# Kernel optimization log

Hardware: AMD Instinct MI355X
Metric: run time of the kernel (lower is better)

Reference implementation:

```python
import jax, jax.numpy as jnp
import numpy as np

D_MODEL = 512
NUM_HEADS = 8
D_K = D_MODEL // NUM_HEADS
SCALE = D_K ** (-0.5)
B, L = 2, 256


def _tropical_linear(x, W, b):
    # max-plus linear: y[..., o] = max_i (x[..., i] + W[o, i]) + b[o]
    # x: (B, L, Din), W: (Dout, Din)
    return jnp.max(x[:, :, None, :] + W[None, None, :, :], axis=-1) + b


def _split_heads(t):
    Bn, Ln, Dn = t.shape
    return t.reshape(Bn, Ln, NUM_HEADS, D_K).transpose(0, 2, 1, 3)  # (B,H,L,dk)


def setup_inputs() -> dict:
    key = jax.random.key(0)
    ks = jax.random.split(key, 8)
    s = 1.0 / np.sqrt(D_MODEL)
    return {
        "x": jax.random.normal(ks[0], (B, L, D_MODEL), jnp.float32),
        "qW": jax.random.normal(ks[1], (D_MODEL, D_MODEL), jnp.float32) * s,
        "qb": jnp.zeros((D_MODEL,), jnp.float32),
        "kW": jax.random.normal(ks[2], (D_MODEL, D_MODEL), jnp.float32) * s,
        "kb": jnp.zeros((D_MODEL,), jnp.float32),
        "vW": jax.random.normal(ks[3], (D_MODEL, D_MODEL), jnp.float32) * s,
        "vb": jnp.zeros((D_MODEL,), jnp.float32),
        "oW": jax.random.normal(ks[4], (D_MODEL, D_MODEL), jnp.float32) * s,
        "ob": jnp.zeros((D_MODEL,), jnp.float32),
        "gW": jnp.zeros((NUM_HEADS, D_MODEL), jnp.float32),  # torch init: zeros
        "gb": jnp.full((NUM_HEADS,), 2.0, jnp.float32),      # torch init: +2.0
        "temp": jnp.ones((NUM_HEADS,), jnp.float32),
    }


def reference(x, qW, qb, kW, kb, vW, vb, oW, ob, gW, gb, temp):
    Bn, Ln, Dn = x.shape
    Q = _split_heads(_tropical_linear(x, qW, qb))  # (B,H,L,dk)
    K = _split_heads(_tropical_linear(x, kW, kb))
    V = _split_heads(x @ vW.T + vb)

    class_scores = jnp.einsum('bhqd,bhkd->bhqk', Q, K) * SCALE
    # tropical max-plus scores: max_d (Q[q,d] + K[k,d])
    trop_scores = jnp.max(Q[:, :, :, None, :] + K[:, :, None, :, :], axis=-1) * SCALE

    g = jax.nn.sigmoid(x @ gW.T + gb)            # (B,L,H)
    g = g.transpose(0, 2, 1)[..., None]          # (B,H,L,1)
    scores = g * trop_scores + (1.0 - g) * class_scores

    # Maslov temperature softmax: per-head learnable temperature
    attn = jax.nn.softmax(scores / temp[None, :, None, None], axis=-1)

    out = jnp.einsum('bhqk,bhkd->bhqd', attn, V)
    out = out.transpose(0, 2, 1, 3).reshape(Bn, Ln, Dn)
    return out @ oW.T + ob, attn
```

## Files before the change

### kernel.cpp

```cpp
#include <hip/hip_runtime.h>
#include <math.h>

#define DM    512
#define LSEQ  256
#define NB    2
#define NH    8
#define DK    64
#define SCALEF 0.125f
#define KC    64

__global__ __launch_bounds__(256) void qkvg_kernel(
    const float* __restrict__ x,
    const float* __restrict__ qW, const float* __restrict__ qb,
    const float* __restrict__ kW, const float* __restrict__ kb,
    const float* __restrict__ vW, const float* __restrict__ vb,
    const float* __restrict__ gW, const float* __restrict__ gb,
    float* __restrict__ Qo, float* __restrict__ Ko,
    float* __restrict__ Vo, float* __restrict__ go)
{
    const int tid = threadIdx.x;
    const int bx  = blockIdx.x;

    if (bx >= 192) {
        const int gx  = bx - 192;
        const int row = gx * 32 + (tid >> 3);
        const int h   = tid & 7;
        const float4* xr = (const float4*)(x  + row * DM);
        const float4* wr = (const float4*)(gW + h  * DM);
        float acc = 0.f;
        #pragma unroll 8
        for (int i = 0; i < DM / 4; ++i) {
            float4 a = xr[i], w = wr[i];
            acc = fmaf(a.x, w.x, acc);
            acc = fmaf(a.y, w.y, acc);
            acc = fmaf(a.z, w.z, acc);
            acc = fmaf(a.w, w.w, acc);
        }
        acc += gb[h];
        go[row * NH + h] = 1.f / (1.f + __expf(-acc));
        return;
    }

    const int rt = bx / 24;
    const int ct = bx % 24;
    const int op = ct >> 3;
    const int row0  = rt * 64;
    const int col0m = (ct & 7) * 64;

    const float* __restrict__ W;
    const float* __restrict__ bias;
    float* __restrict__ out;
    bool trop;
    if      (op == 0) { W = qW; bias = qb; out = Qo; trop = true;  }
    else if (op == 1) { W = kW; bias = kb; out = Ko; trop = true;  }
    else              { W = vW; bias = vb; out = Vo; trop = false; }

    __shared__ float Xs[KC][68];
    __shared__ float Ws[KC][68];

    const int ty = tid >> 4, tx = tid & 15;
    const int sr = tid & 63;
    const int sq = tid >> 6;

    const float* xp = x + (row0  + sr) * DM + sq * 16;
    const float* wp = W + (col0m + sr) * DM + sq * 16;

    float4 xg[4], wg[4];
    #pragma unroll
    for (int i = 0; i < 4; ++i) {
        xg[i] = *(const float4*)(xp + i * 4);
        wg[i] = *(const float4*)(wp + i * 4);
    }

    const float init = trop ? -INFINITY : 0.f;
    float acc[4][4];
    #pragma unroll
    for (int i = 0; i < 4; ++i)
        #pragma unroll
        for (int j = 0; j < 4; ++j) acc[i][j] = init;

    for (int k0 = 0; k0 < DM; k0 += KC) {
        __syncthreads();
        #pragma unroll
        for (int i = 0; i < 4; ++i) {
            const int kk = sq * 16 + i * 4;
            Xs[kk + 0][sr] = xg[i].x;  Xs[kk + 1][sr] = xg[i].y;
            Xs[kk + 2][sr] = xg[i].z;  Xs[kk + 3][sr] = xg[i].w;
            Ws[kk + 0][sr] = wg[i].x;  Ws[kk + 1][sr] = wg[i].y;
            Ws[kk + 2][sr] = wg[i].z;  Ws[kk + 3][sr] = wg[i].w;
        }
        __syncthreads();
        if (k0 + KC < DM) {
            #pragma unroll
            for (int i = 0; i < 4; ++i) {
                xg[i] = *(const float4*)(xp + k0 + KC + i * 4);
                wg[i] = *(const float4*)(wp + k0 + KC + i * 4);
            }
        }
        if (trop) {
            #pragma unroll 4
            for (int kp = 0; kp < KC / 2; ++kp) {
                const int kk = kp * 2;
                float4 x0 = *(const float4*)&Xs[kk    ][ty * 4];
                float4 x1 = *(const float4*)&Xs[kk + 1][ty * 4];
                float4 w0 = *(const float4*)&Ws[kk    ][tx * 4];
                float4 w1 = *(const float4*)&Ws[kk + 1][tx * 4];
                const float xa0[4] = {x0.x, x0.y, x0.z, x0.w};
                const float xa1[4] = {x1.x, x1.y, x1.z, x1.w};
                const float wa0[4] = {w0.x, w0.y, w0.z, w0.w};
                const float wa1[4] = {w1.x, w1.y, w1.z, w1.w};
                #pragma unroll
                for (int i = 0; i < 4; ++i)
                    #pragma unroll
                    for (int j = 0; j < 4; ++j)
                        acc[i][j] = fmaxf(fmaxf(acc[i][j], xa0[i] + wa0[j]),
                                          xa1[i] + wa1[j]);
            }
        } else {
            #pragma unroll 4
            for (int kp = 0; kp < KC / 2; ++kp) {
                const int kk = kp * 2;
                float4 x0 = *(const float4*)&Xs[kk    ][ty * 4];
                float4 x1 = *(const float4*)&Xs[kk + 1][ty * 4];
                float4 w0 = *(const float4*)&Ws[kk    ][tx * 4];
                float4 w1 = *(const float4*)&Ws[kk + 1][tx * 4];
                const float xa0[4] = {x0.x, x0.y, x0.z, x0.w};
                const float xa1[4] = {x1.x, x1.y, x1.z, x1.w};
                const float wa0[4] = {w0.x, w0.y, w0.z, w0.w};
                const float wa1[4] = {w1.x, w1.y, w1.z, w1.w};
                #pragma unroll
                for (int i = 0; i < 4; ++i)
                    #pragma unroll
                    for (int j = 0; j < 4; ++j) {
                        acc[i][j] = fmaf(xa0[i], wa0[j], acc[i][j]);
                        acc[i][j] = fmaf(xa1[i], wa1[j], acc[i][j]);
                    }
            }
        }
    }

    const float4 bv = *(const float4*)&bias[col0m + tx * 4];
    #pragma unroll
    for (int i = 0; i < 4; ++i) {
        const int r = row0 + ty * 4 + i;
        float4 o = make_float4(acc[i][0] + bv.x, acc[i][1] + bv.y,
                               acc[i][2] + bv.z, acc[i][3] + bv.w);
        *(float4*)&out[(size_t)r * DM + col0m + tx * 4] = o;
    }
}

__global__ __launch_bounds__(256) void attn_kernel(
    const float* __restrict__ Q, const float* __restrict__ K,
    const float* __restrict__ V, const float* __restrict__ g,
    const float* __restrict__ temp,
    float* __restrict__ attn_out, float* __restrict__ hout)
{
    const int tid = threadIdx.x;
    const int bh  = blockIdx.y;
    const int b   = bh >> 3, h = bh & 7;
    const int q0  = blockIdx.x * 16;
    const int ty  = tid >> 4, tx = tid & 15;

    __shared__ float Kd[64][68];
    __shared__ float Vs[64][68];
    __shared__ float Ss[16][260];

    const float* qrow = Q + (size_t)(b * LSEQ + q0 + ty) * DM + h * DK;
    float4 qreg[16];
    #pragma unroll
    for (int i = 0; i < 16; ++i) qreg[i] = *(const float4*)(qrow + i * 4);

    const float gq   = g[(b * LSEQ + q0 + ty) * NH + h];
    const float invt = SCALEF / temp[h];

    const int sr = tid & 63;
    const int sq = tid >> 6;

    for (int kt = 0; kt < 4; ++kt) {
        __syncthreads();
        {
            const float* kp = K + (size_t)(b * LSEQ + kt * 64 + sr) * DM
                              + h * DK + sq * 16;
            #pragma unroll
            for (int i = 0; i < 4; ++i) {
                float4 v = *(const float4*)(kp + i * 4);
                const int d = sq * 16 + i * 4;
                Kd[d + 0][sr] = v.x;  Kd[d + 1][sr] = v.y;
                Kd[d + 2][sr] = v.z;  Kd[d + 3][sr] = v.w;
            }
        }
        __syncthreads();
        float d0 = 0.f, d1 = 0.f, d2 = 0.f, d3 = 0.f;
        float t0 = -INFINITY, t1 = -INFINITY, t2 = -INFINITY, t3 = -INFINITY;
        #pragma unroll
        for (int k4 = 0; k4 < 16; ++k4) {
            const float4 q4 = qreg[k4];
            float4 ka = *(const float4*)&Kd[k4 * 4 + 0][tx * 4];
            float4 kb = *(const float4*)&Kd[k4 * 4 + 1][tx * 4];
            float4 kc = *(const float4*)&Kd[k4 * 4 + 2][tx * 4];
            float4 kd = *(const float4*)&Kd[k4 * 4 + 3][tx * 4];
            d0 = fmaf(q4.x, ka.x, d0); d0 = fmaf(q4.y, kb.x, d0);
            d0 = fmaf(q4.z, kc.x, d0); d0 = fmaf(q4.w, kd.x, d0);
            d1 = fmaf(q4.x, ka.y, d1); d1 = fmaf(q4.y, kb.y, d1);
            d1 = fmaf(q4.z, kc.y, d1); d1 = fmaf(q4.w, kd.y, d1);
            d2 = fmaf(q4.x, ka.z, d2); d2 = fmaf(q4.y, kb.z, d2);
            d2 = fmaf(q4.z, kc.z, d2); d2 = fmaf(q4.w, kd.z, d2);
            d3 = fmaf(q4.x, ka.w, d3); d3 = fmaf(q4.y, kb.w, d3);
            d3 = fmaf(q4.z, kc.w, d3); d3 = fmaf(q4.w, kd.w, d3);
            t0 = fmaxf(fmaxf(t0, q4.x + ka.x), q4.y + kb.x);
            t0 = fmaxf(fmaxf(t0, q4.z + kc.x), q4.w + kd.x);
            t1 = fmaxf(fmaxf(t1, q4.x + ka.y), q4.y + kb.y);
            t1 = fmaxf(fmaxf(t1, q4.z + kc.y), q4.w + kd.y);
            t2 = fmaxf(fmaxf(t2, q4.x + ka.z), q4.y + kb.z);
            t2 = fmaxf(fmaxf(t2, q4.z + kc.z), q4.w + kd.z);
            t3 = fmaxf(fmaxf(t3, q4.x + ka.w), q4.y + kb.w);
            t3 = fmaxf(fmaxf(t3, q4.z + kc.w), q4.w + kd.w);
        }
        const float gi = 1.f - gq;
        *(float4*)&Ss[ty][kt * 64 + tx * 4] = make_float4(
            (gq * t0 + gi * d0) * invt, (gq * t1 + gi * d1) * invt,
            (gq * t2 + gi * d2) * invt, (gq * t3 + gi * d3) * invt);
    }
    __syncthreads();

    {
        float m = -INFINITY;
        #pragma unroll 4
        for (int j = 0; j < 16; ++j) m = fmaxf(m, Ss[ty][tx + 16 * j]);
        #pragma unroll
        for (int o = 8; o; o >>= 1) m = fmaxf(m, __shfl_xor(m, o));
        float s = 0.f;
        #pragma unroll 4
        for (int j = 0; j < 16; ++j) {
            const float e = __expf(Ss[ty][tx + 16 * j] - m);
            Ss[ty][tx + 16 * j] = e;
            s += e;
        }
        #pragma unroll
        for (int o = 8; o; o >>= 1) s += __shfl_xor(s, o);
        const float rs = 1.f / s;
        #pragma unroll 4
        for (int j = 0; j < 16; ++j) Ss[ty][tx + 16 * j] *= rs;
    }

    {
        float* dst = attn_out + (size_t)(bh * LSEQ + q0 + ty) * LSEQ;
        #pragma unroll
        for (int j = 0; j < 4; ++j)
            *(float4*)&dst[j * 64 + tx * 4] =
                *(const float4*)&Ss[ty][j * 64 + tx * 4];
    }

    float o0 = 0.f, o1 = 0.f, o2 = 0.f, o3 = 0.f;
    const int vr = tid & 63;
    const int vc = tid >> 6;
    for (int kt = 0; kt < 4; ++kt) {
        __syncthreads();
        {
            const float* vp = V + (size_t)(b * LSEQ + kt * 64 + vr) * DM
                              + h * DK + vc * 16;
            #pragma unroll
            for (int i = 0; i < 4; ++i)
                *(float4*)&Vs[vr][vc * 16 + i * 4] = *(const float4*)(vp + i * 4);
        }
        __syncthreads();
        #pragma unroll 8
        for (int k2 = 0; k2 < 32; ++k2) {
            float2 a2 = *(const float2*)&Ss[ty][kt * 64 + k2 * 2];
            float4 v0 = *(const float4*)&Vs[k2 * 2    ][tx * 4];
            float4 v1 = *(const float4*)&Vs[k2 * 2 + 1][tx * 4];
            o0 = fmaf(a2.x, v0.x, o0); o0 = fmaf(a2.y, v1.x, o0);
            o1 = fmaf(a2.x, v0.y, o1); o1 = fmaf(a2.y, v1.y, o1);
            o2 = fmaf(a2.x, v0.z, o2); o2 = fmaf(a2.y, v1.z, o2);
            o3 = fmaf(a2.x, v0.w, o3); o3 = fmaf(a2.y, v1.w, o3);
        }
    }
    *(float4*)&hout[(size_t)(b * LSEQ + q0 + ty) * DM + h * DK + tx * 4] =
        make_float4(o0, o1, o2, o3);
}

__global__ __launch_bounds__(256) void oproj_kernel(
    const float* __restrict__ hout,
    const float* __restrict__ oW, const float* __restrict__ ob,
    float* __restrict__ out)
{
    const int tid = threadIdx.x;
    const int bx  = blockIdx.x;
    const int row0 = (bx >> 4) * 32;
    const int col0 = (bx & 15) * 32;

    __shared__ float Xs[KC][36];
    __shared__ float Ws[KC][36];

    const int ty = tid >> 4, tx = tid & 15;
    const int sr = tid & 31;
    const int sq = tid >> 5;

    const float* xp = hout + (size_t)(row0 + sr) * DM + sq * 8;
    const float* wp = oW   + (size_t)(col0 + sr) * DM + sq * 8;

    float4 xg[2], wg[2];
    #pragma unroll
    for (int i = 0; i < 2; ++i) {
        xg[i] = *(const float4*)(xp + i * 4);
        wg[i] = *(const float4*)(wp + i * 4);
    }

    float a00 = 0.f, a01 = 0.f, a10 = 0.f, a11 = 0.f;

    for (int k0 = 0; k0 < DM; k0 += KC) {
        __syncthreads();
        #pragma unroll
        for (int i = 0; i < 2; ++i) {
            const int kk = sq * 8 + i * 4;
            Xs[kk + 0][sr] = xg[i].x;  Xs[kk + 1][sr] = xg[i].y;
            Xs[kk + 2][sr] = xg[i].z;  Xs[kk + 3][sr] = xg[i].w;
            Ws[kk + 0][sr] = wg[i].x;  Ws[kk + 1][sr] = wg[i].y;
            Ws[kk + 2][sr] = wg[i].z;  Ws[kk + 3][sr] = wg[i].w;
        }
        __syncthreads();
        if (k0 + KC < DM) {
            #pragma unroll
            for (int i = 0; i < 2; ++i) {
                xg[i] = *(const float4*)(xp + k0 + KC + i * 4);
                wg[i] = *(const float4*)(wp + k0 + KC + i * 4);
            }
        }
        #pragma unroll 8
        for (int kk = 0; kk < KC; ++kk) {
            float2 xv = *(const float2*)&Xs[kk][ty * 2];
            float2 wv = *(const float2*)&Ws[kk][tx * 2];
            a00 = fmaf(xv.x, wv.x, a00);
            a01 = fmaf(xv.x, wv.y, a01);
            a10 = fmaf(xv.y, wv.x, a10);
            a11 = fmaf(xv.y, wv.y, a11);
        }
    }

    const int r0 = row0 + ty * 2, c0 = col0 + tx * 2;
    const float b0 = ob[c0], b1 = ob[c0 + 1];
    *(float2*)&out[(size_t)r0       * DM + c0] = make_float2(a00 + b0, a01 + b1);
    *(float2*)&out[(size_t)(r0 + 1) * DM + c0] = make_float2(a10 + b0, a11 + b1);
}

extern "C" void kernel_launch(void* const* d_in, const int* in_sizes, int n_in,
                              void* d_out, int out_size, void* d_ws, size_t ws_size,
                              hipStream_t stream)
{
    const float* x    = (const float*)d_in[0];
    const float* qW   = (const float*)d_in[1];
    const float* qb   = (const float*)d_in[2];
    const float* kW   = (const float*)d_in[3];
    const float* kb   = (const float*)d_in[4];
    const float* vW   = (const float*)d_in[5];
    const float* vb   = (const float*)d_in[6];
    const float* oW   = (const float*)d_in[7];
    const float* ob   = (const float*)d_in[8];
    const float* gW   = (const float*)d_in[9];
    const float* gb   = (const float*)d_in[10];
    const float* temp = (const float*)d_in[11];

    float* out      = (float*)d_out;
    float* attn_out = out + NB * LSEQ * DM;

    float* ws   = (float*)d_ws;
    float* Qo   = ws;
    float* Ko   = Qo + NB * LSEQ * DM;
    float* Vo   = Ko + NB * LSEQ * DM;
    float* go   = Vo + NB * LSEQ * DM;
    float* hout = go + NB * LSEQ * NH;

    qkvg_kernel<<<dim3(208), 256, 0, stream>>>(
        x, qW, qb, kW, kb, vW, vb, gW, gb, Qo, Ko, Vo, go);
    attn_kernel<<<dim3(16, 16), 256, 0, stream>>>(
        Qo, Ko, Vo, go, temp, attn_out, hout);
    oproj_kernel<<<dim3(256), 256, 0, stream>>>(
        hout, oW, ob, out);
}
```

Measured before the change: 154.0 us.

## Split-K the QKV and output projections and widen attention blocks

```diff
diff --git a/kernel.cpp b/kernel.cpp
--- a/kernel.cpp
+++ b/kernel.cpp
@@ -11,18 +11,16 @@
 
 __global__ __launch_bounds__(256) void qkvg_kernel(
     const float* __restrict__ x,
-    const float* __restrict__ qW, const float* __restrict__ qb,
-    const float* __restrict__ kW, const float* __restrict__ kb,
-    const float* __restrict__ vW, const float* __restrict__ vb,
+    const float* __restrict__ qW, const float* __restrict__ kW,
+    const float* __restrict__ vW,
     const float* __restrict__ gW, const float* __restrict__ gb,
-    float* __restrict__ Qo, float* __restrict__ Ko,
-    float* __restrict__ Vo, float* __restrict__ go)
+    float* __restrict__ P1, float* __restrict__ go)
 {
     const int tid = threadIdx.x;
     const int bx  = blockIdx.x;
 
-    if (bx >= 192) {
-        const int gx  = bx - 192;
+    if (bx >= 768) {
+        const int gx  = bx - 768;
         const int row = gx * 32 + (tid >> 3);
         const int h   = tid & 7;
         const float4* xr = (const float4*)(x  + row * DM);
@@ -41,19 +39,17 @@
         return;
     }
 
-    const int rt = bx / 24;
-    const int ct = bx % 24;
+    const int ks = bx & 3;
+    const int t  = bx >> 2;
+    const int rt = t / 24;
+    const int ct = t % 24;
     const int op = ct >> 3;
     const int row0  = rt * 64;
     const int col0m = (ct & 7) * 64;
-
-    const float* __restrict__ W;
-    const float* __restrict__ bias;
-    float* __restrict__ out;
-    bool trop;
-    if      (op == 0) { W = qW; bias = qb; out = Qo; trop = true;  }
-    else if (op == 1) { W = kW; bias = kb; out = Ko; trop = true;  }
-    else              { W = vW; bias = vb; out = Vo; trop = false; }
+    const int kbase = ks * 128;
+
+    const float* __restrict__ W = (op == 0) ? qW : (op == 1) ? kW : vW;
+    const bool trop = (op < 2);
 
     __shared__ float Xs[KC][68];
     __shared__ float Ws[KC][68];
@@ -62,8 +58,8 @@
     const int sr = tid & 63;
     const int sq = tid >> 6;
 
-    const float* xp = x + (row0  + sr) * DM + sq * 16;
-    const float* wp = W + (col0m + sr) * DM + sq * 16;
+    const float* xp = x + (row0  + sr) * DM + kbase + sq * 16;
+    const float* wp = W + (col0m + sr) * DM + kbase + sq * 16;
 
     float4 xg[4], wg[4];
     #pragma unroll
@@ -79,7 +75,8 @@
         #pragma unroll
         for (int j = 0; j < 4; ++j) acc[i][j] = init;
 
-    for (int k0 = 0; k0 < DM; k0 += KC) {
+    #pragma unroll
+    for (int k0 = 0; k0 < 128; k0 += KC) {
         __syncthreads();
         #pragma unroll
         for (int i = 0; i < 4; ++i) {
@@ -90,11 +87,11 @@
             Ws[kk + 2][sr] = wg[i].z;  Ws[kk + 3][sr] = wg[i].w;
         }
         __syncthreads();
-        if (k0 + KC < DM) {
+        if (k0 + KC < 128) {
             #pragma unroll
             for (int i = 0; i < 4; ++i) {
-                xg[i] = *(const float4*)(xp + k0 + KC + i * 4);
-                wg[i] = *(const float4*)(wp + k0 + KC + i * 4);
+                xg[i] = *(const float4*)(xp + KC + i * 4);
+                wg[i] = *(const float4*)(wp + KC + i * 4);
             }
         }
         if (trop) {
@@ -139,17 +136,57 @@
         }
     }
 
-    const float4 bv = *(const float4*)&bias[col0m + tx * 4];
+    const int gcol = op * 512 + col0m + tx * 4;
     #pragma unroll
     for (int i = 0; i < 4; ++i) {
         const int r = row0 + ty * 4 + i;
-        float4 o = make_float4(acc[i][0] + bv.x, acc[i][1] + bv.y,
-                               acc[i][2] + bv.z, acc[i][3] + bv.w);
-        *(float4*)&out[(size_t)r * DM + col0m + tx * 4] = o;
-    }
-}
-
-__global__ __launch_bounds__(256) void attn_kernel(
+        *(float4*)&P1[((size_t)ks * 512 + r) * 1536 + gcol] =
+            make_float4(acc[i][0], acc[i][1], acc[i][2], acc[i][3]);
+    }
+}
+
+__global__ __launch_bounds__(256) void qkv_reduce_kernel(
+    const float* __restrict__ P1,
+    const float* __restrict__ qb, const float* __restrict__ kb,
+    const float* __restrict__ vb,
+    float* __restrict__ Qo, float* __restrict__ Ko, float* __restrict__ Vo)
+{
+    const int e   = blockIdx.x * 256 + threadIdx.x;
+    const int row = e / 384;
+    const int col = (e % 384) * 4;
+    const size_t base = (size_t)row * 1536 + col;
+
+    float4 p0 = *(const float4*)&P1[base];
+    float4 p1 = *(const float4*)&P1[base +  786432];
+    float4 p2 = *(const float4*)&P1[base + 1572864];
+    float4 p3 = *(const float4*)&P1[base + 2359296];
+
+    if (col < 1024) {
+        float4 r = make_float4(
+            fmaxf(fmaxf(p0.x, p1.x), fmaxf(p2.x, p3.x)),
+            fmaxf(fmaxf(p0.y, p1.y), fmaxf(p2.y, p3.y)),
+            fmaxf(fmaxf(p0.z, p1.z), fmaxf(p2.z, p3.z)),
+            fmaxf(fmaxf(p0.w, p1.w), fmaxf(p2.w, p3.w)));
+        if (col < 512) {
+            float4 b = *(const float4*)&qb[col];
+            r.x += b.x; r.y += b.y; r.z += b.z; r.w += b.w;
+            *(float4*)&Qo[(size_t)row * DM + col] = r;
+        } else {
+            float4 b = *(const float4*)&kb[col - 512];
+            r.x += b.x; r.y += b.y; r.z += b.z; r.w += b.w;
+            *(float4*)&Ko[(size_t)row * DM + col - 512] = r;
+        }
+    } else {
+        float4 b = *(const float4*)&vb[col - 1024];
+        float4 r = make_float4(p0.x + p1.x + p2.x + p3.x + b.x,
+                               p0.y + p1.y + p2.y + p3.y + b.y,
+                               p0.z + p1.z + p2.z + p3.z + b.z,
+                               p0.w + p1.w + p2.w + p3.w + b.w);
+        *(float4*)&Vo[(size_t)row * DM + col - 1024] = r;
+    }
+}
+
+__global__ __launch_bounds__(512) void attn_kernel(
     const float* __restrict__ Q, const float* __restrict__ K,
     const float* __restrict__ V, const float* __restrict__ g,
     const float* __restrict__ temp,
@@ -159,17 +196,19 @@
     const int bh  = blockIdx.y;
     const int b   = bh >> 3, h = bh & 7;
     const int q0  = blockIdx.x * 16;
-    const int ty  = tid >> 4, tx = tid & 15;
-
+    const int ty  = tid >> 5;
+    const int tx  = tid & 31;
+
+    __shared__ float Qs[16][68];
     __shared__ float Kd[64][68];
-    __shared__ float Vs[64][68];
+    __shared__ float Vs[2][64][68];
     __shared__ float Ss[16][260];
 
-    const float* qrow = Q + (size_t)(b * LSEQ + q0 + ty) * DM + h * DK;
-    float4 qreg[16];
-    #pragma unroll
-    for (int i = 0; i < 16; ++i) qreg[i] = *(const float4*)(qrow + i * 4);
-
+    if (tid < 256) {
+        const int r = tid >> 4, c = (tid & 15) * 4;
+        *(float4*)&Qs[r][c] =
+            *(const float4*)&Q[(size_t)(b * LSEQ + q0 + r) * DM + h * DK + c];
+    }
     const float gq   = g[(b * LSEQ + q0 + ty) * NH + h];
     const float invt = SCALEF / temp[h];
 
@@ -180,167 +219,204 @@
         __syncthreads();
         {
             const float* kp = K + (size_t)(b * LSEQ + kt * 64 + sr) * DM
-                              + h * DK + sq * 16;
+                              + h * DK + sq * 8;
             #pragma unroll
-            for (int i = 0; i < 4; ++i) {
+            for (int i = 0; i < 2; ++i) {
                 float4 v = *(const float4*)(kp + i * 4);
-                const int d = sq * 16 + i * 4;
+                const int d = sq * 8 + i * 4;
                 Kd[d + 0][sr] = v.x;  Kd[d + 1][sr] = v.y;
                 Kd[d + 2][sr] = v.z;  Kd[d + 3][sr] = v.w;
             }
         }
         __syncthreads();
-        float d0 = 0.f, d1 = 0.f, d2 = 0.f, d3 = 0.f;
-        float t0 = -INFINITY, t1 = -INFINITY, t2 = -INFINITY, t3 = -INFINITY;
+        float d0 = 0.f, d1 = 0.f;
+        float t0 = -INFINITY, t1 = -INFINITY;
         #pragma unroll
         for (int k4 = 0; k4 < 16; ++k4) {
-            const float4 q4 = qreg[k4];
-            float4 ka = *(const float4*)&Kd[k4 * 4 + 0][tx * 4];
-            float4 kb = *(const float4*)&Kd[k4 * 4 + 1][tx * 4];
-            float4 kc = *(const float4*)&Kd[k4 * 4 + 2][tx * 4];
-            float4 kd = *(const float4*)&Kd[k4 * 4 + 3][tx * 4];
+            const float4 q4 = *(const float4*)&Qs[ty][k4 * 4];
+            float2 ka = *(const float2*)&Kd[k4 * 4 + 0][tx * 2];
+            float2 kb = *(const float2*)&Kd[k4 * 4 + 1][tx * 2];
+            float2 kc = *(const float2*)&Kd[k4 * 4 + 2][tx * 2];
+            float2 kd = *(const float2*)&Kd[k4 * 4 + 3][tx * 2];
             d0 = fmaf(q4.x, ka.x, d0); d0 = fmaf(q4.y, kb.x, d0);
             d0 = fmaf(q4.z, kc.x, d0); d0 = fmaf(q4.w, kd.x, d0);
             d1 = fmaf(q4.x, ka.y, d1); d1 = fmaf(q4.y, kb.y, d1);
             d1 = fmaf(q4.z, kc.y, d1); d1 = fmaf(q4.w, kd.y, d1);
-            d2 = fmaf(q4.x, ka.z, d2); d2 = fmaf(q4.y, kb.z, d2);
-            d2 = fmaf(q4.z, kc.z, d2); d2 = fmaf(q4.w, kd.z, d2);
-            d3 = fmaf(q4.x, ka.w, d3); d3 = fmaf(q4.y, kb.w, d3);
-            d3 = fmaf(q4.z, kc.w, d3); d3 = fmaf(q4.w, kd.w, d3);
             t0 = fmaxf(fmaxf(t0, q4.x + ka.x), q4.y + kb.x);
             t0 = fmaxf(fmaxf(t0, q4.z + kc.x), q4.w + kd.x);
             t1 = fmaxf(fmaxf(t1, q4.x + ka.y), q4.y + kb.y);
             t1 = fmaxf(fmaxf(t1, q4.z + kc.y), q4.w + kd.y);
-            t2 = fmaxf(fmaxf(t2, q4.x + ka.z), q4.y + kb.z);
-            t2 = fmaxf(fmaxf(t2, q4.z + kc.z), q4.w + kd.z);
-            t3 = fmaxf(fmaxf(t3, q4.x + ka.w), q4.y + kb.w);
-            t3 = fmaxf(fmaxf(t3, q4.z + kc.w), q4.w + kd.w);
         }
         const float gi = 1.f - gq;
-        *(float4*)&Ss[ty][kt * 64 + tx * 4] = make_float4(
-            (gq * t0 + gi * d0) * invt, (gq * t1 + gi * d1) * invt,
-            (gq * t2 + gi * d2) * invt, (gq * t3 + gi * d3) * invt);
+        *(float2*)&Ss[ty][kt * 64 + tx * 2] = make_float2(
+            (gq * t0 + gi * d0) * invt, (gq * t1 + gi * d1) * invt);
     }
     __syncthreads();
 
     {
         float m = -INFINITY;
-        #pragma unroll 4
-        for (int j = 0; j < 16; ++j) m = fmaxf(m, Ss[ty][tx + 16 * j]);
-        #pragma unroll
-        for (int o = 8; o; o >>= 1) m = fmaxf(m, __shfl_xor(m, o));
+        #pragma unroll
+        for (int j = 0; j < 8; ++j) m = fmaxf(m, Ss[ty][tx + 32 * j]);
+        #pragma unroll
+        for (int o = 16; o; o >>= 1) m = fmaxf(m, __shfl_xor(m, o));
         float s = 0.f;
-        #pragma unroll 4
-        for (int j = 0; j < 16; ++j) {
-            const float e = __expf(Ss[ty][tx + 16 * j] - m);
-            Ss[ty][tx + 16 * j] = e;
+        #pragma unroll
+        for (int j = 0; j < 8; ++j) {
+            const float e = __expf(Ss[ty][tx + 32 * j] - m);
+            Ss[ty][tx + 32 * j] = e;
             s += e;
         }
         #pragma unroll
-        for (int o = 8; o; o >>= 1) s += __shfl_xor(s, o);
+        for (int o = 16; o; o >>= 1) s += __shfl_xor(s, o);
         const float rs = 1.f / s;
-        #pragma unroll 4
-        for (int j = 0; j < 16; ++j) Ss[ty][tx + 16 * j] *= rs;
-    }
+        #pragma unroll
+        for (int j = 0; j < 8; ++j) Ss[ty][tx + 32 * j] *= rs;
+    }
+    __syncthreads();
 
     {
-        float* dst = attn_out + (size_t)(bh * LSEQ + q0 + ty) * LSEQ;
-        #pragma unroll
-        for (int j = 0; j < 4; ++j)
-            *(float4*)&dst[j * 64 + tx * 4] =
-                *(const float4*)&Ss[ty][j * 64 + tx * 4];
-    }
-
+        float* dst = attn_out + (size_t)(bh * LSEQ + q0) * LSEQ;
+        #pragma unroll
+        for (int i = 0; i < 2; ++i) {
+            const int f   = i * 2048 + tid * 4;
+            const int row = f >> 8, col = f & 255;
+            *(float4*)&dst[f] = *(const float4*)&Ss[row][col];
+        }
+    }
+
+    const int kh = tid >> 8;
+    const int bb = tid & 255;
+    const int r  = bb >> 4;
+    const int d4 = bb & 15;
     float o0 = 0.f, o1 = 0.f, o2 = 0.f, o3 = 0.f;
-    const int vr = tid & 63;
-    const int vc = tid >> 6;
-    for (int kt = 0; kt < 4; ++kt) {
+
+    const int vr    = tid & 63;
+    const int vslot = tid >> 6;
+
+    for (int p = 0; p < 2; ++p) {
         __syncthreads();
         {
-            const float* vp = V + (size_t)(b * LSEQ + kt * 64 + vr) * DM
-                              + h * DK + vc * 16;
+            const int tile = vslot >> 2;
+            const int tidx = tile ? (2 + p) : p;
+            const float* vp = V + (size_t)(b * LSEQ + tidx * 64 + vr) * DM
+                              + h * DK + (vslot & 3) * 16;
             #pragma unroll
             for (int i = 0; i < 4; ++i)
-                *(float4*)&Vs[vr][vc * 16 + i * 4] = *(const float4*)(vp + i * 4);
-        }
-        __syncthreads();
-        #pragma unroll 8
-        for (int k2 = 0; k2 < 32; ++k2) {
-            float2 a2 = *(const float2*)&Ss[ty][kt * 64 + k2 * 2];
-            float4 v0 = *(const float4*)&Vs[k2 * 2    ][tx * 4];
-            float4 v1 = *(const float4*)&Vs[k2 * 2 + 1][tx * 4];
-            o0 = fmaf(a2.x, v0.x, o0); o0 = fmaf(a2.y, v1.x, o0);
-            o1 = fmaf(a2.x, v0.y, o1); o1 = fmaf(a2.y, v1.y, o1);
-            o2 = fmaf(a2.x, v0.z, o2); o2 = fmaf(a2.y, v1.z, o2);
-            o3 = fmaf(a2.x, v0.w, o3); o3 = fmaf(a2.y, v1.w, o3);
-        }
-    }
-    *(float4*)&hout[(size_t)(b * LSEQ + q0 + ty) * DM + h * DK + tx * 4] =
-        make_float4(o0, o1, o2, o3);
+                *(float4*)&Vs[tile][vr][(vslot & 3) * 16 + i * 4] =
+                    *(const float4*)(vp + i * 4);
+        }
+        __syncthreads();
+        const int kt = kh * 2 + p;
+        #pragma unroll 4
+        for (int k4 = 0; k4 < 16; ++k4) {
+            float4 a  = *(const float4*)&Ss[r][kt * 64 + k4 * 4];
+            float4 v0 = *(const float4*)&Vs[kh][k4 * 4 + 0][d4 * 4];
+            float4 v1 = *(const float4*)&Vs[kh][k4 * 4 + 1][d4 * 4];
+            float4 v2 = *(const float4*)&Vs[kh][k4 * 4 + 2][d4 * 4];
+            float4 v3 = *(const float4*)&Vs[kh][k4 * 4 + 3][d4 * 4];
+            o0 = fmaf(a.x, v0.x, o0); o0 = fmaf(a.y, v1.x, o0);
+            o0 = fmaf(a.z, v2.x, o0); o0 = fmaf(a.w, v3.x, o0);
+            o1 = fmaf(a.x, v0.y, o1); o1 = fmaf(a.y, v1.y, o1);
+            o1 = fmaf(a.z, v2.y, o1); o1 = fmaf(a.w, v3.y, o1);
+            o2 = fmaf(a.x, v0.z, o2); o2 = fmaf(a.y, v1.z, o2);
+            o2 = fmaf(a.z, v2.z, o2); o2 = fmaf(a.w, v3.z, o2);
+            o3 = fmaf(a.x, v0.w, o3); o3 = fmaf(a.y, v1.w, o3);
+            o3 = fmaf(a.z, v2.w, o3); o3 = fmaf(a.w, v3.w, o3);
+        }
+    }
+    __syncthreads();
+    if (kh == 1)
+        *(float4*)&Kd[r][d4 * 4] = make_float4(o0, o1, o2, o3);
+    __syncthreads();
+    if (kh == 0) {
+        float4 po = *(const float4*)&Kd[r][d4 * 4];
+        *(float4*)&hout[(size_t)(b * LSEQ + q0 + r) * DM + h * DK + d4 * 4] =
+            make_float4(o0 + po.x, o1 + po.y, o2 + po.z, o3 + po.w);
+    }
 }
 
 __global__ __launch_bounds__(256) void oproj_kernel(
     const float* __restrict__ hout,
-    const float* __restrict__ oW, const float* __restrict__ ob,
-    float* __restrict__ out)
+    const float* __restrict__ oW,
+    float* __restrict__ P2)
 {
     const int tid = threadIdx.x;
     const int bx  = blockIdx.x;
-    const int row0 = (bx >> 4) * 32;
-    const int col0 = (bx & 15) * 32;
-
-    __shared__ float Xs[KC][36];
-    __shared__ float Ws[KC][36];
+    const int ks  = bx & 7;
+    const int t   = bx >> 3;
+    const int row0 = (t >> 3) * 64;
+    const int col0 = (t & 7) * 64;
+    const int kbase = ks * 64;
+
+    __shared__ float Xs[KC][68];
+    __shared__ float Ws[KC][68];
 
     const int ty = tid >> 4, tx = tid & 15;
-    const int sr = tid & 31;
-    const int sq = tid >> 5;
-
-    const float* xp = hout + (size_t)(row0 + sr) * DM + sq * 8;
-    const float* wp = oW   + (size_t)(col0 + sr) * DM + sq * 8;
-
-    float4 xg[2], wg[2];
-    #pragma unroll
-    for (int i = 0; i < 2; ++i) {
-        xg[i] = *(const float4*)(xp + i * 4);
-        wg[i] = *(const float4*)(wp + i * 4);
-    }
-
-    float a00 = 0.f, a01 = 0.f, a10 = 0.f, a11 = 0.f;
-
-    for (int k0 = 0; k0 < DM; k0 += KC) {
-        __syncthreads();
-        #pragma unroll
-        for (int i = 0; i < 2; ++i) {
-            const int kk = sq * 8 + i * 4;
-            Xs[kk + 0][sr] = xg[i].x;  Xs[kk + 1][sr] = xg[i].y;
-            Xs[kk + 2][sr] = xg[i].z;  Xs[kk + 3][sr] = xg[i].w;
-            Ws[kk + 0][sr] = wg[i].x;  Ws[kk + 1][sr] = wg[i].y;
-            Ws[kk + 2][sr] = wg[i].z;  Ws[kk + 3][sr] = wg[i].w;
-        }
-        __syncthreads();
-        if (k0 + KC < DM) {
+    const int sr = tid & 63;
+    const int sq = tid >> 6;
+
+    {
+        const float* xp = hout + (size_t)(row0 + sr) * DM + kbase + sq * 16;
+        const float* wp = oW   + (size_t)(col0 + sr) * DM + kbase + sq * 16;
+        #pragma unroll
+        for (int i = 0; i < 4; ++i) {
+            float4 xv = *(const float4*)(xp + i * 4);
+            float4 wv = *(const float4*)(wp + i * 4);
+            const int kk = sq * 16 + i * 4;
+            Xs[kk + 0][sr] = xv.x;  Xs[kk + 1][sr] = xv.y;
+            Xs[kk + 2][sr] = xv.z;  Xs[kk + 3][sr] = xv.w;
+            Ws[kk + 0][sr] = wv.x;  Ws[kk + 1][sr] = wv.y;
+            Ws[kk + 2][sr] = wv.z;  Ws[kk + 3][sr] = wv.w;
+        }
+    }
+    __syncthreads();
+
+    float acc[4][4] = {};
+    #pragma unroll 4
+    for (int kp = 0; kp < KC / 2; ++kp) {
+        const int kk = kp * 2;
+        float4 x0 = *(const float4*)&Xs[kk    ][ty * 4];
+        float4 x1 = *(const float4*)&Xs[kk + 1][ty * 4];
+        float4 w0 = *(const float4*)&Ws[kk    ][tx * 4];
+        float4 w1 = *(const float4*)&Ws[kk + 1][tx * 4];
+        const float xa0[4] = {x0.x, x0.y, x0.z, x0.w};
+        const float xa1[4] = {x1.x, x1.y, x1.z, x1.w};
+        const float wa0[4] = {w0.x, w0.y, w0.z, w0.w};
+        const float wa1[4] = {w1.x, w1.y, w1.z, w1.w};
+        #pragma unroll
+        for (int i = 0; i < 4; ++i)
             #pragma unroll
-            for (int i = 0; i < 2; ++i) {
-                xg[i] = *(const float4*)(xp + k0 + KC + i * 4);
-                wg[i] = *(const float4*)(wp + k0 + KC + i * 4);
+            for (int j = 0; j < 4; ++j) {
+                acc[i][j] = fmaf(xa0[i], wa0[j], acc[i][j]);
+                acc[i][j] = fmaf(xa1[i], wa1[j], acc[i][j]);
             }
-        }
-        #pragma unroll 8
-        for (int kk = 0; kk < KC; ++kk) {
-            float2 xv = *(const float2*)&Xs[kk][ty * 2];
-            float2 wv = *(const float2*)&Ws[kk][tx * 2];
-            a00 = fmaf(xv.x, wv.x, a00);
-            a01 = fmaf(xv.x, wv.y, a01);
-            a10 = fmaf(xv.y, wv.x, a10);
-            a11 = fmaf(xv.y, wv.y, a11);
-        }
-    }
-
-    const int r0 = row0 + ty * 2, c0 = col0 + tx * 2;
-    const float b0 = ob[c0], b1 = ob[c0 + 1];
-    *(float2*)&out[(size_t)r0       * DM + c0] = make_float2(a00 + b0, a01 + b1);
-    *(float2*)&out[(size_t)(r0 + 1) * DM + c0] = make_float2(a10 + b0, a11 + b1);
+    }
+
+    #pragma unroll
+    for (int i = 0; i < 4; ++i) {
+        const int r = row0 + ty * 4 + i;
+        *(float4*)&P2[((size_t)ks * 512 + r) * 512 + col0 + tx * 4] =
+            make_float4(acc[i][0], acc[i][1], acc[i][2], acc[i][3]);
+    }
+}
+
+__global__ __launch_bounds__(256) void oproj_reduce_kernel(
+    const float* __restrict__ P2, const float* __restrict__ ob,
+    float* __restrict__ out)
+{
+    const int e   = blockIdx.x * 256 + threadIdx.x;
+    const int row = e >> 7;
+    const int col = (e & 127) * 4;
+    const size_t base = (size_t)row * 512 + col;
+
+    float4 b = *(const float4*)&ob[col];
+    float4 r = b;
+    #pragma unroll
+    for (int s = 0; s < 8; ++s) {
+        float4 p = *(const float4*)&P2[base + (size_t)s * 262144];
+        r.x += p.x; r.y += p.y; r.z += p.z; r.w += p.w;
+    }
+    *(float4*)&out[base] = r;
 }
 
 extern "C" void kernel_launch(void* const* d_in, const int* in_sizes, int n_in,
@@ -369,11 +445,17 @@
     float* Vo   = Ko + NB * LSEQ * DM;
     float* go   = Vo + NB * LSEQ * DM;
     float* hout = go + NB * LSEQ * NH;
-
-    qkvg_kernel<<<dim3(208), 256, 0, stream>>>(
-        x, qW, qb, kW, kb, vW, vb, gW, gb, Qo, Ko, Vo, go);
-    attn_kernel<<<dim3(16, 16), 256, 0, stream>>>(
+    float* P1   = hout + NB * LSEQ * DM;
+    float* P2   = P1;
+
+    qkvg_kernel<<<dim3(784), 256, 0, stream>>>(
+        x, qW, kW, vW, gW, gb, P1, go);
+    qkv_reduce_kernel<<<dim3(768), 256, 0, stream>>>(
+        P1, qb, kb, vb, Qo, Ko, Vo);
+    attn_kernel<<<dim3(16, 16), 512, 0, stream>>>(
         Qo, Ko, Vo, go, temp, attn_out, hout);
-    oproj_kernel<<<dim3(256), 256, 0, stream>>>(
-        hout, oW, ob, out);
-}
+    oproj_kernel<<<dim3(512), 256, 0, stream>>>(
+        hout, oW, P2);
+    oproj_reduce_kernel<<<dim3(256), 256, 0, stream>>>(
+        P2, ob, out);
+}
```

After: 141.6 us. 1.09x faster.
